# Performance work log

Measured on AMD Instinct MI355X. Metric: run time of the kernel, lower is better.

Reference implementation:

```python
import jax, jax.numpy as jnp
import numpy as np

BETA = 0.25
NUM_VECTORS = 1024
LATENT_DIM = 256

def setup_inputs() -> dict:
    key = jax.random.key(0)
    k1, k2 = jax.random.split(key)
    z = jax.random.normal(k1, (32, LATENT_DIM, 64, 64), dtype=jnp.float32)
    # embedding initialized uniform(-1/K, 1/K) as in the torch module
    emb = jax.random.uniform(k2, (NUM_VECTORS, LATENT_DIM), dtype=jnp.float32,
                             minval=-1.0 / NUM_VECTORS, maxval=1.0 / NUM_VECTORS)
    return {"z": z, "emb": emb}

def reference(z, emb):
    B, C, H, W = z.shape
    zp = jnp.transpose(z, (0, 2, 3, 1))            # [B,H,W,C]
    zf = zp.reshape(-1, C)                          # [N,C]
    # pairwise squared L2 distances: ||z||^2 + ||e||^2 - 2 z e^T -> [N,K]
    d = (jnp.sum(zf * zf, axis=-1, keepdims=True)
         + jnp.sum(emb * emb, axis=-1)
         - 2.0 * (zf @ emb.T))
    idx = jnp.argmin(d, axis=1)                     # [N]
    zq = emb[idx].reshape(B, H, W, C)               # gather + reshape
    # loss exactly as source: mse(zq, sg(z)) - beta * mse(z, sg(zq))
    loss = (jnp.mean((zq - jax.lax.stop_gradient(zp)) ** 2)
            - BETA * jnp.mean((zp - jax.lax.stop_gradient(zq)) ** 2))
    # straight-through estimator
    zq_st = zp + jax.lax.stop_gradient(zq - zp)
    zq_out = jnp.transpose(zq_st, (0, 3, 1, 2))     # back to [B,C,H,W]
    return zq_out, idx, loss
```

## Files before the change

### kernel.cpp

```cpp
#include <hip/hip_runtime.h>
#include <stdint.h>

#define B_   32
#define C_   256
#define HW_  4096
#define N_   131072
#define K_   1024

typedef __attribute__((ext_vector_type(8))) short bf16x8;
typedef __attribute__((ext_vector_type(4))) float f32x4;

__device__ __forceinline__ unsigned short f2bf(float f) {
    unsigned int x = __float_as_uint(f);
    return (unsigned short)((x + 0x7FFFu + ((x >> 16) & 1u)) >> 16);
}
__device__ __forceinline__ float bf2f(unsigned short h) {
    return __uint_as_float(((unsigned int)h) << 16);
}

#define GLD16(g, l) __builtin_amdgcn_global_load_lds((const __attribute__((address_space(1))) void*)(g), \
                        (__attribute__((address_space(3))) void*)(l), 16, 0, 0)

__global__ void ee_kernel(const float* __restrict__ emb, float* __restrict__ ee) {
#pragma clang fp contract(off)
    int k = blockIdx.x * blockDim.x + threadIdx.x;
    if (k >= K_) return;
    const float* e = emb + (size_t)k * C_;
    float res = 0.f;
    for (int h = 0; h < 2; ++h) {
        float r[8];
        #pragma unroll
        for (int j = 0; j < 8; ++j) { float v = e[h*128 + j]; r[j] = v * v; }
        for (int i = 8; i < 128; i += 8) {
            #pragma unroll
            for (int j = 0; j < 8; ++j) { float v = e[h*128 + i + j]; r[j] += v * v; }
        }
        float s = ((r[0] + r[1]) + (r[2] + r[3])) + ((r[4] + r[5]) + (r[6] + r[7]));
        res += s;
    }
    ee[k] = res;
}

__global__ void zz_kernel(const float* __restrict__ z, float* __restrict__ zz) {
#pragma clang fp contract(off)
    int n = blockIdx.x * blockDim.x + threadIdx.x;
    if (n >= N_) return;
    int b = n >> 12, hw = n & 4095;
    const float* zp = z + (size_t)b * C_ * HW_ + hw;
    float res = 0.f;
    for (int h = 0; h < 2; ++h) {
        float r[8];
        #pragma unroll
        for (int j = 0; j < 8; ++j) { float v = zp[(size_t)(h*128 + j) * HW_]; r[j] = v * v; }
        for (int i = 8; i < 128; i += 8) {
            #pragma unroll
            for (int j = 0; j < 8; ++j) { float v = zp[(size_t)(h*128 + i + j) * HW_]; r[j] += v * v; }
        }
        float s = ((r[0] + r[1]) + (r[2] + r[3])) + ((r[4] + r[5]) + (r[6] + r[7]));
        res += s;
    }
    zz[n] = res;
}

__global__ void esplit_kernel(const float* __restrict__ emb,
                              unsigned short* __restrict__ eh, unsigned short* __restrict__ el) {
    int t = blockIdx.x * 256 + threadIdx.x;
    int k = t >> 5, c8 = (t & 31) * 8;
    const float* src = emb + (size_t)k * C_ + c8;
    unsigned short hb[8], lb[8];
    #pragma unroll
    for (int i = 0; i < 8; ++i) {
        float f = src[i];
        unsigned short h = f2bf(f);
        hb[i] = h; lb[i] = f2bf(f - bf2f(h));
    }
    size_t off = (size_t)k * C_ + c8;
    *(uint4*)&eh[off] = *(uint4*)hb;
    *(uint4*)&el[off] = *(uint4*)lb;
}

__global__ void zsplit_kernel(const float* __restrict__ z,
                              unsigned short* __restrict__ zh, unsigned short* __restrict__ zl) {
    __shared__ float t[64][65];
    int blk = blockIdx.x;
    int b = blk >> 8, ct = (blk >> 6) & 3, ht = blk & 63;
    int tid = threadIdx.x;
    int hw = tid & 63, c0 = tid >> 6;
    const float* src = z + ((size_t)b * C_ + ct * 64) * HW_ + ht * 64;
    #pragma unroll
    for (int k = 0; k < 16; ++k) {
        int c = k * 4 + c0;
        t[c][hw] = src[(size_t)c * HW_ + hw];
    }
    __syncthreads();
    int hw2 = tid >> 2, cs = (tid & 3) * 16;
    size_t off = ((size_t)b * HW_ + ht * 64 + hw2) * C_ + ct * 64 + cs;
    unsigned short hb[16], lb[16];
    #pragma unroll
    for (int i = 0; i < 16; ++i) {
        float f = t[cs + i][hw2];
        unsigned short h = f2bf(f);
        hb[i] = h; lb[i] = f2bf(f - bf2f(h));
    }
    *(uint4*)&zh[off]     = *(uint4*)&hb[0];
    *(uint4*)&zh[off + 8] = *(uint4*)&hb[8];
    *(uint4*)&zl[off]     = *(uint4*)&lb[0];
    *(uint4*)&zl[off + 8] = *(uint4*)&lb[8];
}

#define INS3(T, P) do { uint32_t _p = (P); \
    if (_p < T[2]) { if (_p < T[1]) { T[2] = T[1]; \
        if (_p < T[0]) { T[1] = T[0]; T[0] = _p; } else T[1] = _p; } else T[2] = _p; } } while (0)

__launch_bounds__(256)
__global__ void mfma_argmin_kernel(const unsigned short* __restrict__ zh, const unsigned short* __restrict__ zl,
                                   const unsigned short* __restrict__ eh, const unsigned short* __restrict__ el,
                                   const float* __restrict__ ee, uint32_t* __restrict__ top3) {
    __shared__ unsigned short Ah[128*32], Al[128*32], Bh[128*32], Bl[128*32];
    __shared__ float eesh[K_];
    __shared__ uint32_t red[128][2][3];

    const int tid = threadIdx.x;
    const int lane = tid & 63, wave = tid >> 6;
    const int wr = wave >> 1, wc = wave & 1;
    const int row0 = blockIdx.x * 128;

    for (int i = tid; i < K_; i += 256) eesh[i] = ee[i];

    uint32_t t3[16][3];
    #pragma unroll
    for (int s = 0; s < 16; ++s) { t3[s][0] = 0xFFFFFFFFu; t3[s][1] = 0xFFFFFFFFu; t3[s][2] = 0xFFFFFFFFu; }

    const int lr  = lane >> 2;
    const int lc8 = (lane & 3) * 8;
    const int fr  = lane & 15;
    const int fk  = (lane >> 4) * 8;
    const int rb  = wave * 32;

    __syncthreads();

    for (int kt = 0; kt < 8; ++kt) {
        f32x4 acc[4][4];
        #pragma unroll
        for (int m = 0; m < 4; ++m)
            #pragma unroll
            for (int n = 0; n < 4; ++n) acc[m][n] = (f32x4){0.f, 0.f, 0.f, 0.f};

        for (int c0 = 0; c0 < C_; c0 += 32) {
            size_t ga0 = (size_t)(row0 + rb + lr) * C_ + c0 + lc8;
            size_t ga1 = ga0 + (size_t)16 * C_;
            size_t gb0 = (size_t)(kt * 128 + rb + lr) * C_ + c0 + lc8;
            size_t gb1 = gb0 + (size_t)16 * C_;
            GLD16(zh + ga0, &Ah[(rb +  0) * 32]);
            GLD16(zh + ga1, &Ah[(rb + 16) * 32]);
            GLD16(zl + ga0, &Al[(rb +  0) * 32]);
            GLD16(zl + ga1, &Al[(rb + 16) * 32]);
            GLD16(eh + gb0, &Bh[(rb +  0) * 32]);
            GLD16(eh + gb1, &Bh[(rb + 16) * 32]);
            GLD16(el + gb0, &Bl[(rb +  0) * 32]);
            GLD16(el + gb1, &Bl[(rb + 16) * 32]);
            __syncthreads();

            bf16x8 ah[4], al4[4], bh[4], bl4[4];
            #pragma unroll
            for (int m = 0; m < 4; ++m) {
                int r = wr * 64 + m * 16 + fr;
                ah[m]  = *(const bf16x8*)&Ah[r * 32 + fk];
                al4[m] = *(const bf16x8*)&Al[r * 32 + fk];
            }
            #pragma unroll
            for (int n = 0; n < 4; ++n) {
                int r = wc * 64 + n * 16 + fr;
                bh[n]  = *(const bf16x8*)&Bh[r * 32 + fk];
                bl4[n] = *(const bf16x8*)&Bl[r * 32 + fk];
            }
            #pragma unroll
            for (int m = 0; m < 4; ++m)
                #pragma unroll
                for (int n = 0; n < 4; ++n) {
                    acc[m][n] = __builtin_amdgcn_mfma_f32_16x16x32_bf16(ah[m],  bh[n],  acc[m][n], 0, 0, 0);
                    acc[m][n] = __builtin_amdgcn_mfma_f32_16x16x32_bf16(ah[m],  bl4[n], acc[m][n], 0, 0, 0);
                    acc[m][n] = __builtin_amdgcn_mfma_f32_16x16x32_bf16(al4[m], bh[n],  acc[m][n], 0, 0, 0);
                }
            __syncthreads();
        }

        #pragma unroll
        for (int n = 0; n < 4; ++n) {
            int col = kt * 128 + wc * 64 + n * 16 + fr;
            float eev = eesh[col];
            #pragma unroll
            for (int m = 0; m < 4; ++m) {
                #pragma unroll
                for (int j = 0; j < 4; ++j) {
                    float d = eev - 2.0f * acc[m][n][j];
                    uint32_t bbits = __float_as_uint(d);
                    uint32_t u = bbits ^ (0x80000000u | (uint32_t)((int32_t)bbits >> 31));
                    uint32_t p = (u & 0xFFFFFC00u) | (uint32_t)col;
                    INS3(t3[m * 4 + j], p);
                }
            }
        }
    }

    #pragma unroll
    for (int st = 1; st < 16; st <<= 1) {
        #pragma unroll
        for (int s = 0; s < 16; ++s) {
            uint32_t q0 = __shfl_xor(t3[s][0], st, 64);
            uint32_t q1 = __shfl_xor(t3[s][1], st, 64);
            uint32_t q2 = __shfl_xor(t3[s][2], st, 64);
            INS3(t3[s], q0); INS3(t3[s], q1); INS3(t3[s], q2);
        }
    }
    if ((lane & 15) == 0) {
        int g = lane >> 4;
        #pragma unroll
        for (int m = 0; m < 4; ++m)
            #pragma unroll
            for (int j = 0; j < 4; ++j) {
                int r = wr * 64 + m * 16 + g * 4 + j;
                int s = m * 4 + j;
                red[r][wc][0] = t3[s][0]; red[r][wc][1] = t3[s][1]; red[r][wc][2] = t3[s][2];
            }
    }
    __syncthreads();
    if (tid < 128) {
        uint32_t a0 = red[tid][0][0], a1 = red[tid][0][1], a2 = red[tid][0][2];
        uint32_t b0 = red[tid][1][0], b1 = red[tid][1][1], b2 = red[tid][1][2];
        uint32_t o0, o1, o2;
        if (a0 <= b0) { o0 = a0;
            if (a1 <= b0) { o1 = a1; o2 = (a2 < b0 ? a2 : b0); }
            else          { o1 = b0; o2 = (a1 < b1 ? a1 : b1); }
        } else { o0 = b0;
            if (b1 <= a0) { o1 = b1; o2 = (b2 < a0 ? b2 : a0); }
            else          { o1 = a0; o2 = (a1 < b1 ? a1 : b1); }
        }
        uint32_t* dst = top3 + (size_t)(row0 + tid) * 3;
        dst[0] = o0; dst[1] = o1; dst[2] = o2;
    }
}

__global__ void refine_kernel(const float* __restrict__ z, const float* __restrict__ emb,
                              const float* __restrict__ zz, const float* __restrict__ ee,
                              const uint32_t* __restrict__ top3,
                              int* __restrict__ idx_i, float* __restrict__ idx_f) {
    int n = blockIdx.x * 256 + threadIdx.x;
    int b = n >> 12, hw = n & 4095;
    int c0 = (int)(top3[(size_t)n * 3 + 0] & 0x3FFu);
    int c1 = (int)(top3[(size_t)n * 3 + 1] & 0x3FFu);
    int c2 = (int)(top3[(size_t)n * 3 + 2] & 0x3FFu);
    int t;
    if (c1 < c0) { t = c0; c0 = c1; c1 = t; }
    if (c2 < c1) { t = c1; c1 = c2; c2 = t; }
    if (c1 < c0) { t = c0; c0 = c1; c1 = t; }
    const float* zp = z + (size_t)b * C_ * HW_ + hw;
    const float* e0 = emb + (size_t)c0 * C_;
    const float* e1 = emb + (size_t)c1 * C_;
    const float* e2 = emb + (size_t)c2 * C_;
    float a0 = 0.f, a1 = 0.f, a2 = 0.f;
    for (int c = 0; c < C_; ++c) {
        float zv = zp[(size_t)c * HW_];
        a0 = fmaf(zv, e0[c], a0);
        a1 = fmaf(zv, e1[c], a1);
        a2 = fmaf(zv, e2[c], a2);
    }
    float zzr = zz[n];
    float A0 = zzr + ee[c0]; float d0 = A0 - 2.0f * a0;
    float A1 = zzr + ee[c1]; float d1 = A1 - 2.0f * a1;
    float A2 = zzr + ee[c2]; float d2 = A2 - 2.0f * a2;
    float bv = d0; int bi = c0;
    if (c1 != c0 && d1 < bv) { bv = d1; bi = c1; }
    if (c2 != c1 && c2 != c0 && d2 < bv) { bv = d2; bi = c2; }
    idx_i[n] = bi;
    idx_f[n] = (float)bi;
}

__global__ void gather_kernel(const float* __restrict__ z, const float* __restrict__ emb,
                              const int* __restrict__ idx, float* __restrict__ zq,
                              float* __restrict__ partials) {
#pragma clang fp contract(off)
    const long long TOT = (long long)N_ * (C_/4);
    float ls = 0.f;
    for (long long g = (long long)blockIdx.x * blockDim.x + threadIdx.x; g < TOT;
         g += (long long)gridDim.x * blockDim.x) {
        int c4 = (int)(g >> 17);
        int n  = (int)(g & (N_ - 1));
        int b = n >> 12, hw = n & 4095;
        int j = idx[n];
        float4 e4 = *(const float4*)&emb[(size_t)j * C_ + c4*4];
        size_t base = (size_t)b * C_ * HW_ + (size_t)(c4*4) * HW_ + hw;
        float zv, df;
        zv = z[base + 0*HW_]; df = e4.x - zv; zq[base + 0*HW_] = zv + df; ls += df*df;
        zv = z[base + 1*HW_]; df = e4.y - zv; zq[base + 1*HW_] = zv + df; ls += df*df;
        zv = z[base + 2*HW_]; df = e4.z - zv; zq[base + 2*HW_] = zv + df; ls += df*df;
        zv = z[base + 3*HW_]; df = e4.w - zv; zq[base + 3*HW_] = zv + df; ls += df*df;
    }
    __shared__ float sred[256];
    sred[threadIdx.x] = ls;
    __syncthreads();
    for (int s = 128; s > 0; s >>= 1) {
        if (threadIdx.x < s) sred[threadIdx.x] += sred[threadIdx.x + s];
        __syncthreads();
    }
    if (threadIdx.x == 0) partials[blockIdx.x] = sred[0];
}

__global__ void finalize_kernel(const float* __restrict__ partials, int nparts,
                                float* __restrict__ loss_out) {
    __shared__ float sred[256];
    float s = 0.f;
    for (int i = threadIdx.x; i < nparts; i += 256) s += partials[i];
    sred[threadIdx.x] = s; __syncthreads();
    for (int st = 128; st > 0; st >>= 1) {
        if (threadIdx.x < st) sred[threadIdx.x] += sred[threadIdx.x + st];
        __syncthreads();
    }
    if (threadIdx.x == 0) {
        float m = sred[0] / 33554432.0f;
        *loss_out = m - 0.25f * m;
    }
}

extern "C" void kernel_launch(void* const* d_in, const int* in_sizes, int n_in,
                              void* d_out, int out_size, void* d_ws, size_t ws_size,
                              hipStream_t stream) {
    const float* z   = (const float*)d_in[0];
    const float* emb = (const float*)d_in[1];
    float* out   = (float*)d_out;
    float* zq    = out;
    float* idx_f = out + (size_t)N_ * C_;
    float* loss  = idx_f + N_;

    unsigned short* zh = (unsigned short*)d_out;
    unsigned short* zl = zh + (size_t)N_ * C_;

    float*     zz       = (float*)d_ws;
    float*     ee       = zz + N_;
    int*       idx_i    = (int*)(ee + K_);
    uint32_t*  top3     = (uint32_t*)(idx_i + N_);
    float*     partials = (float*)(top3 + (size_t)3 * N_);
    unsigned short* eh  = (unsigned short*)(partials + 2048);
    unsigned short* el  = eh + (size_t)K_ * C_;

    esplit_kernel<<<128, 256, 0, stream>>>(emb, eh, el);
    ee_kernel<<<(K_ + 255)/256, 256, 0, stream>>>(emb, ee);
    zsplit_kernel<<<8192, 256, 0, stream>>>(z, zh, zl);
    zz_kernel<<<N_/256, 256, 0, stream>>>(z, zz);
    mfma_argmin_kernel<<<N_/128, 256, 0, stream>>>(zh, zl, eh, el, ee, top3);
    refine_kernel<<<N_/256, 256, 0, stream>>>(z, emb, zz, ee, top3, idx_i, idx_f);
    gather_kernel<<<2048, 256, 0, stream>>>(z, emb, idx_i, zq, partials);
    finalize_kernel<<<1, 256, 0, stream>>>(partials, 2048, loss);
}
```

Baseline: 799.6 us.

## Fuse z-norm into refine kernel and swizzle MFMA LDS tile layout

Drops the standalone zz_kernel and computes each row's squared norm inside refine_kernel, in the same pass that reads z for the three candidate dot products, keeping the same 8-way summation order so the result matches bitwise. This removes one full read of z (about 128 MB) and a launch. The refine loop now loads the embedding rows as float4. The MFMA argmin kernel also XOR-swizzles its LDS column offsets to reduce bank conflicts; that only stays correct if the store and fragment-read indices agree.

```diff
diff --git a/kernel.cpp b/kernel.cpp
--- a/kernel.cpp
+++ b/kernel.cpp
@@ -41,27 +41,6 @@
     ee[k] = res;
 }
 
-__global__ void zz_kernel(const float* __restrict__ z, float* __restrict__ zz) {
-#pragma clang fp contract(off)
-    int n = blockIdx.x * blockDim.x + threadIdx.x;
-    if (n >= N_) return;
-    int b = n >> 12, hw = n & 4095;
-    const float* zp = z + (size_t)b * C_ * HW_ + hw;
-    float res = 0.f;
-    for (int h = 0; h < 2; ++h) {
-        float r[8];
-        #pragma unroll
-        for (int j = 0; j < 8; ++j) { float v = zp[(size_t)(h*128 + j) * HW_]; r[j] = v * v; }
-        for (int i = 8; i < 128; i += 8) {
-            #pragma unroll
-            for (int j = 0; j < 8; ++j) { float v = zp[(size_t)(h*128 + i + j) * HW_]; r[j] += v * v; }
-        }
-        float s = ((r[0] + r[1]) + (r[2] + r[3])) + ((r[4] + r[5]) + (r[6] + r[7]));
-        res += s;
-    }
-    zz[n] = res;
-}
-
 __global__ void esplit_kernel(const float* __restrict__ emb,
                               unsigned short* __restrict__ eh, unsigned short* __restrict__ el) {
     int t = blockIdx.x * 256 + threadIdx.x;
@@ -132,9 +111,9 @@
     for (int s = 0; s < 16; ++s) { t3[s][0] = 0xFFFFFFFFu; t3[s][1] = 0xFFFFFFFFu; t3[s][2] = 0xFFFFFFFFu; }
 
     const int lr  = lane >> 2;
-    const int lc8 = (lane & 3) * 8;
+    const int lc8 = (((lane & 3) ^ ((lr >> 1) & 3)) * 8);
     const int fr  = lane & 15;
-    const int fk  = (lane >> 4) * 8;
+    const int fk  = (((lane >> 4) ^ ((fr >> 1) & 3)) * 8);
     const int rb  = wave * 32;
 
     __syncthreads();
@@ -241,10 +220,11 @@
     }
 }
 
+__launch_bounds__(256)
 __global__ void refine_kernel(const float* __restrict__ z, const float* __restrict__ emb,
-                              const float* __restrict__ zz, const float* __restrict__ ee,
-                              const uint32_t* __restrict__ top3,
+                              const float* __restrict__ ee, const uint32_t* __restrict__ top3,
                               int* __restrict__ idx_i, float* __restrict__ idx_f) {
+#pragma clang fp contract(off)
     int n = blockIdx.x * 256 + threadIdx.x;
     int b = n >> 12, hw = n & 4095;
     int c0 = (int)(top3[(size_t)n * 3 + 0] & 0x3FFu);
@@ -255,17 +235,49 @@
     if (c2 < c1) { t = c1; c1 = c2; c2 = t; }
     if (c1 < c0) { t = c0; c0 = c1; c1 = t; }
     const float* zp = z + (size_t)b * C_ * HW_ + hw;
-    const float* e0 = emb + (size_t)c0 * C_;
-    const float* e1 = emb + (size_t)c1 * C_;
-    const float* e2 = emb + (size_t)c2 * C_;
+    const float4* e0 = (const float4*)(emb + (size_t)c0 * C_);
+    const float4* e1 = (const float4*)(emb + (size_t)c1 * C_);
+    const float4* e2 = (const float4*)(emb + (size_t)c2 * C_);
     float a0 = 0.f, a1 = 0.f, a2 = 0.f;
-    for (int c = 0; c < C_; ++c) {
-        float zv = zp[(size_t)c * HW_];
-        a0 = fmaf(zv, e0[c], a0);
-        a1 = fmaf(zv, e1[c], a1);
-        a2 = fmaf(zv, e2[c], a2);
-    }
-    float zzr = zz[n];
+    float zzr = 0.f;
+
+    #pragma unroll
+    for (int half = 0; half < 2; ++half) {
+        float r[8];
+        #pragma unroll 2
+        for (int c4l = 0; c4l < 2; ++c4l) {
+            int c4 = half * 32 + c4l;
+            float4 v0 = e0[c4], v1 = e1[c4], v2 = e2[c4];
+            #pragma unroll
+            for (int i = 0; i < 4; ++i) {
+                int c = c4 * 4 + i;
+                float zv = zp[(size_t)c * HW_];
+                r[c4l * 4 + i] = zv * zv;
+                a0 = fmaf(zv, ((const float*)&v0)[i], a0);
+                a1 = fmaf(zv, ((const float*)&v1)[i], a1);
+                a2 = fmaf(zv, ((const float*)&v2)[i], a2);
+            }
+        }
+        #pragma unroll 6
+        for (int c4l = 2; c4l < 32; ++c4l) {
+            int c4 = half * 32 + c4l;
+            float4 v0 = e0[c4], v1 = e1[c4], v2 = e2[c4];
+            #pragma unroll
+            for (int i = 0; i < 4; ++i) {
+                int c = c4 * 4 + i;
+                float zv = zp[(size_t)c * HW_];
+                float sq = zv * zv;
+                int j = (c4l * 4 + i) & 7;
+                r[j] = r[j] + sq;
+                a0 = fmaf(zv, ((const float*)&v0)[i], a0);
+                a1 = fmaf(zv, ((const float*)&v1)[i], a1);
+                a2 = fmaf(zv, ((const float*)&v2)[i], a2);
+            }
+        }
+        float s = ((r[0] + r[1]) + (r[2] + r[3])) + ((r[4] + r[5]) + (r[6] + r[7]));
+        zzr = zzr + s;
+    }
+
     float A0 = zzr + ee[c0]; float d0 = A0 - 2.0f * a0;
     float A1 = zzr + ee[c1]; float d1 = A1 - 2.0f * a1;
     float A2 = zzr + ee[c2]; float d2 = A2 - 2.0f * a2;
@@ -335,8 +347,7 @@
     unsigned short* zh = (unsigned short*)d_out;
     unsigned short* zl = zh + (size_t)N_ * C_;
 
-    float*     zz       = (float*)d_ws;
-    float*     ee       = zz + N_;
+    float*     ee       = (float*)d_ws;
     int*       idx_i    = (int*)(ee + K_);
     uint32_t*  top3     = (uint32_t*)(idx_i + N_);
     float*     partials = (float*)(top3 + (size_t)3 * N_);
@@ -346,9 +357,8 @@
     esplit_kernel<<<128, 256, 0, stream>>>(emb, eh, el);
     ee_kernel<<<(K_ + 255)/256, 256, 0, stream>>>(emb, ee);
     zsplit_kernel<<<8192, 256, 0, stream>>>(z, zh, zl);
-    zz_kernel<<<N_/256, 256, 0, stream>>>(z, zz);
     mfma_argmin_kernel<<<N_/128, 256, 0, stream>>>(zh, zl, eh, el, ee, top3);
-    refine_kernel<<<N_/256, 256, 0, stream>>>(z, emb, zz, ee, top3, idx_i, idx_f);
+    refine_kernel<<<N_/256, 256, 0, stream>>>(z, emb, ee, top3, idx_i, idx_f);
     gather_kernel<<<2048, 256, 0, stream>>>(z, emb, idx_i, zq, partials);
     finalize_kernel<<<1, 256, 0, stream>>>(partials, 2048, loss);
 }
```

Result: faster. 719.3 us (-10.0%).
